# Kernel optimization log

Measured on AMD Instinct MI355X. Metric: run time of the kernel, lower is better.

## Reference

```python
import jax, jax.numpy as jnp
from jax import lax
import numpy as np

NUM_EMBEDDINGS = 8192
EMBEDDING_DIM = 256
COMMITMENT_COST = 0.25


def setup_inputs() -> dict:
    key = jax.random.key(0)
    k1, k2 = jax.random.split(key)
    z = jax.random.normal(k1, (16, EMBEDDING_DIM, 32, 32), dtype=jnp.float32)
    codebook = jax.random.uniform(
        k2, (NUM_EMBEDDINGS, EMBEDDING_DIM), dtype=jnp.float32,
        minval=-1.0 / NUM_EMBEDDINGS, maxval=1.0 / NUM_EMBEDDINGS)
    return {"z": z, "codebook": codebook}


def reference(z, codebook):
    B, C, H, W = z.shape  # C == embedding_dim
    zp = jnp.transpose(z, (0, 2, 3, 1))          # [B, H, W, C]
    z_flat = zp.reshape(-1, C)                    # [N, C], N = B*H*W
    # squared-distance via ||z||^2 + ||e||^2 - 2 z.e
    z2 = jnp.sum(z_flat * z_flat, axis=1, keepdims=True)   # [N, 1]
    e2 = jnp.sum(codebook * codebook, axis=1)               # [K]
    ez = z_flat @ codebook.T                                # [N, K]
    distances = z2 + e2 - 2.0 * ez                          # [N, K]
    e_indices = jnp.argmin(distances, axis=1)               # [N]
    z_q = codebook[e_indices]                               # [N, C]
    # Faithfully reproduce the original's mislabeled unpack:
    # torch does B, D, H, W = z.shape on the BHWC tensor, then
    # z_q.view(B, H, W, D).permute(0, 3, 1, 2) == reshape(B, W, C, H) -> (0,3,1,2)
    z_q = jnp.transpose(z_q.reshape(B, W, C, H), (0, 3, 1, 2))  # [B, H, W, C]
    commitment_loss = jnp.mean((lax.stop_gradient(zp) - z_q) ** 2)
    codebook_loss = jnp.mean((zp - lax.stop_gradient(z_q)) ** 2)
    loss = codebook_loss + COMMITMENT_COST * commitment_loss
    z_q_st = zp + lax.stop_gradient(z_q - zp)   # straight-through, [B, H, W, C]
    return z_q_st, loss, e_indices
```

## Files before the change

kernel.cpp:

```cpp
#include <hip/hip_runtime.h>
#include <stdint.h>

#define NROWS 16384
#define KENT  8192
#define CDIM  256
#define NELEM 4194304

#define ZSCALE 22.0f
#define ESCALE 1040384.0f
#define MARGIN_INT 4096
#define SBIAS 4194304


typedef int v4i __attribute__((ext_vector_type(4)));

__device__ inline int q8(float x, float s) {
    int v = __float2int_rn(x * s);
    return v < -127 ? -127 : (v > 127 ? 127 : v);
}
__device__ inline unsigned pk4(int a, int b, int c, int d) {
    return (a & 255) | ((b & 255) << 8) | ((c & 255) << 16) | ((d & 255) << 24);
}
__device__ inline unsigned umax_(unsigned a, unsigned b) { return a > b ? a : b; }
__device__ inline unsigned umin_(unsigned a, unsigned b) { return a < b ? a : b; }
__device__ inline void gload_lds16(const void* g, void* l) {
    __builtin_amdgcn_global_load_lds(
        (const __attribute__((address_space(1))) void*)g,
        (__attribute__((address_space(3))) void*)l, 16, 0, 0);
}

__global__ __launch_bounds__(128) void vq_prep(
        const float* __restrict__ z, const float* __restrict__ cb,
        float* __restrict__ z2w, char* __restrict__ zbi8,
        char* __restrict__ cbbi8, float* __restrict__ loss_out) {
    const int t = threadIdx.x;
    const int bid = blockIdx.x;

    if (bid >= 256) {
        const int p = bid - 256, n0 = p * 128;
        char* dst = cbbi8 + p * 32768;
        const float* src = cb + (n0 + t) * 256;
#pragma unroll
        for (int q = 0; q < 16; ++q) {
            float4 a = *(const float4*)(src + q * 16);
            float4 b = *(const float4*)(src + q * 16 + 4);
            float4 c = *(const float4*)(src + q * 16 + 8);
            float4 d = *(const float4*)(src + q * 16 + 12);
            uint4 v;
            v.x = pk4(q8(a.x,ESCALE), q8(a.y,ESCALE), q8(a.z,ESCALE), q8(a.w,ESCALE));
            v.y = pk4(q8(b.x,ESCALE), q8(b.y,ESCALE), q8(b.z,ESCALE), q8(b.w,ESCALE));
            v.z = pk4(q8(c.x,ESCALE), q8(c.y,ESCALE), q8(c.z,ESCALE), q8(c.w,ESCALE));
            v.w = pk4(q8(d.x,ESCALE), q8(d.y,ESCALE), q8(d.z,ESCALE), q8(d.w,ESCALE));
            *(uint4*)&dst[(q * 128 + t) * 16] = v;
        }
        if (p == 0 && t == 0) loss_out[0] = 0.f;
        return;
    }

    __shared__ float s64[64];
    const int r = t & 63;
    const int blk = t >> 6;
    const int n = bid * 64 + r;
    const int b = n >> 10, hw = n & 1023;
    const float* base = z + b * 262144 + hw;

    const int p = n >> 7, rp = n & 127;
    char* dst = zbi8 + p * 32768;

    float t0[16], p01[16], p0123[16], C[16];

#pragma unroll
    for (int j = 0; j < 8; ++j) {
        float a[16];
#pragma unroll
        for (int L = 0; L < 16; ++L)
            a[L] = base[(blk * 128 + L + 16 * j) * 1024];
        int qb[16];
#pragma unroll
        for (int L = 0; L < 16; ++L) {
            qb[L] = q8(a[L], ZSCALE);
            float sq = a[L] * a[L];
            asm volatile("" : "+v"(sq));
            if (j == 0 || j == 2 || j == 4 || j == 6) t0[L] = sq;
            else if (j == 1) p01[L] = t0[L] + sq;
            else if (j == 3) p0123[L] = p01[L] + (t0[L] + sq);
            else if (j == 5) p01[L] = t0[L] + sq;
            else             C[L] = p0123[L] + (p01[L] + (t0[L] + sq));
        }
        uint4 v;
        v.x = pk4(qb[0], qb[1], qb[2], qb[3]);
        v.y = pk4(qb[4], qb[5], qb[6], qb[7]);
        v.z = pk4(qb[8], qb[9], qb[10], qb[11]);
        v.w = pk4(qb[12], qb[13], qb[14], qb[15]);
        *(uint4*)&dst[((blk * 8 + j) * 128 + rp) * 16] = v;
    }
    float t8[8];
#pragma unroll
    for (int L = 0; L < 8; ++L) t8[L] = C[L] + C[L + 8];
    float t4[4];
#pragma unroll
    for (int L = 0; L < 4; ++L) t4[L] = t8[L] + t8[L + 4];
    float t2a = t4[0] + t4[2];
    float t2b = t4[1] + t4[3];
    float bs = t2a + t2b;

    if (blk == 1) s64[r] = bs;
    __syncthreads();
    if (blk == 0) z2w[n] = bs + s64[r];
}

__global__ __launch_bounds__(256, 4) void vq_gemm(
        const char* __restrict__ zbi8,
        const char* __restrict__ cbbi8,
        unsigned long long* __restrict__ gstats) {
    __shared__ __align__(16) char smem[32768];

    const int tid = threadIdx.x;
    const int w = tid >> 6, l = tid & 63;
    const int q4 = l >> 4, cl = l & 15;
    const int mw = w & 1, nw = w >> 1;

    const unsigned bx = blockIdx.x;
    const unsigned xcd = bx & 7, local = bx >> 3;
    const unsigned png = local >> 8;
    const unsigned rem = local & 255;
    const unsigned pm = (rem >> 4) * 8 + xcd;
    const unsigned pn = png * 16 + (rem & 15);

    const char* Ab = zbi8 + pm * 32768;
    const char* Bb = cbbi8 + pn * 32768;

#pragma unroll
    for (int u = 0; u < 8; ++u)
        gload_lds16(Ab + u * 4096 + tid * 16, smem + u * 4096 + (w << 10));

    const char* abase = Bb + (q4 * 128 + mw * 64 + cl) * 16;
    v4i af[4], afn[4];
#pragma unroll
    for (int i = 0; i < 4; ++i)
        af[i] = *(const v4i*)(abase + i * 256);

    const unsigned vb = ((unsigned)SBIAS << 6) + (unsigned)(q4 * 4);

    v4i acc[4][4];
    __syncthreads();

#pragma unroll
    for (int kt = 0; kt < 4; ++kt) {
        v4i bfl[4];
#pragma unroll
        for (int j = 0; j < 4; ++j)
            bfl[j] = *(const v4i*)(smem + kt * 8192 + q4 * 2048
                                        + nw * 1024 + j * 256 + cl * 16);
        if (kt < 3) {
#pragma unroll
            for (int i = 0; i < 4; ++i)
                afn[i] = *(const v4i*)(abase + (kt + 1) * 8192 + i * 256);
        }
#pragma unroll
        for (int i = 0; i < 4; ++i)
#pragma unroll
            for (int j = 0; j < 4; ++j) {
                if (kt == 0)
                    acc[i][j] = __builtin_amdgcn_mfma_i32_16x16x64_i8(
                        af[i], bfl[j], (v4i)0, 0, 0, 0);
                else
                    acc[i][j] = __builtin_amdgcn_mfma_i32_16x16x64_i8(
                        af[i], bfl[j], acc[i][j], 0, 0, 0);
            }
#pragma unroll
        for (int i = 0; i < 4; ++i) af[i] = afn[i];
    }

    unsigned long long* gs = gstats + (pn * 2 + (unsigned)mw) * 16384u
                                    + pm * 128u + (unsigned)(nw * 64);
#pragma unroll
    for (int jj = 0; jj < 4; ++jj) {
        unsigned m1[8], m2[8];
#pragma unroll
        for (int i = 0; i < 4; ++i)
#pragma unroll
            for (int gp = 0; gp < 2; ++gp) {
                unsigned pa = ((unsigned)acc[i][jj][2 * gp] << 6)
                              + vb + (unsigned)(i * 16 + 2 * gp);
                unsigned pb = ((unsigned)acc[i][jj][2 * gp + 1] << 6)
                              + vb + (unsigned)(i * 16 + 2 * gp + 1);
                m1[i * 2 + gp] = umax_(pa, pb);
                m2[i * 2 + gp] = umin_(pa, pb);
            }
#pragma unroll
        for (int s = 4; s >= 1; s >>= 1)
#pragma unroll
            for (int u = 0; u < 4; ++u) {
                if (u < s) {
                    unsigned a1 = m1[u], a2 = m2[u];
                    unsigned b1 = m1[u + s], b2 = m2[u + s];
                    m1[u] = umax_(a1, b1);
                    m2[u] = umax_(umin_(a1, b1), umax_(a2, b2));
                }
            }
        unsigned t1 = m1[0], t2 = m2[0];
#pragma unroll
        for (int off = 16; off <= 32; off <<= 1) {
            unsigned o1 = (unsigned)__shfl_xor((int)t1, off);
            unsigned o2 = (unsigned)__shfl_xor((int)t2, off);
            t2 = umax_(umax_(t2, o2), umin_(t1, o1));
            t1 = umax_(t1, o1);
        }
        if (q4 == 0)
            gs[jj * 16 + cl] =
                ((unsigned long long)t1 << 32) | (unsigned long long)t2;
    }
}

__global__ __launch_bounds__(256) void vq_finalize(
        const float* __restrict__ z, const float* __restrict__ cb,
        const float* __restrict__ z2w,
        const unsigned long long* __restrict__ gstats,
        float* __restrict__ out, float* __restrict__ out_idx) {
    __shared__ float zs[32][32];
    __shared__ unsigned pmax[8][32];
    __shared__ int thrL[32];
    __shared__ unsigned candL[512];
    __shared__ unsigned blkcnt;
    __shared__ unsigned long long bestL[32];
    __shared__ float tile[32 * 257];

    const int t = threadIdx.x;
    const int bid = blockIdx.x;
    const int n0 = bid * 32;
    const int b = bid >> 5, j = bid & 31;
    const int hw0 = j * 32;
    const int r = t & 31, gc = t >> 5;

    unsigned long long e[16];
    unsigned m = 0;
#pragma unroll
    for (int g2 = 0; g2 < 16; ++g2) {
        e[g2] = gstats[(size_t)(gc * 16 + g2) * 16384u + (unsigned)(n0 + r)];
        m = umax_(m, (unsigned)(e[g2] >> 32));
    }
    pmax[gc][r] = m;
    if (t == 0) blkcnt = 0;
    __syncthreads();
    if (t < 32) {
        unsigned mm = 0;
#pragma unroll
        for (int g = 0; g < 8; ++g) mm = umax_(mm, pmax[g][t]);
        thrL[t] = (int)(mm >> 6) - MARGIN_INT;
        bestL[t] = ~0ull;
    }
    __syncthreads();

    {
        int th = thrL[r];
#pragma unroll
        for (int g2 = 0; g2 < 16; ++g2) {
            unsigned p1 = (unsigned)(e[g2] >> 32), p2 = (unsigned)e[g2];
            unsigned kb = (unsigned)(gc * 16 + g2) * 64u;
            if ((int)(p1 >> 6) >= th) {
                unsigned pos = atomicAdd(&blkcnt, 1u);
                if (pos < 512u)
                    candL[pos] = ((unsigned)r << 13) | (kb + (p1 & 63u));
            }
            if ((int)(p2 >> 6) >= th) {
                unsigned pos = atomicAdd(&blkcnt, 1u);
                if (pos < 512u)
                    candL[pos] = ((unsigned)r << 13) | (kb + (p2 & 63u));
            }
        }
    }
    __syncthreads();
    int ns = (int)(blkcnt < 512u ? blkcnt : 512u);

    for (int base = 0; base < ns; base += 256) {
        bool active = base + t < ns;
        int rr0 = 0, k = 0;
        if (active) {
            unsigned v = candL[base + t];
            rr0 = v >> 13; k = v & 8191;
        }
        float sacc = 0.f;
        for (int ch = 0; ch < 8; ++ch) {
            __syncthreads();
            {
                int rr = t & 31, cc2 = t >> 5;
#pragma unroll
                for (int u = 0; u < 4; ++u) {
                    int cc = u * 8 + cc2;
                    zs[cc][rr] = z[b * 262144 + (ch * 32 + cc) * 1024 + hw0 + rr];
                }
            }
            __syncthreads();
            if (active) {
                const float4* cbp = (const float4*)(cb + k * 256 + ch * 32);
                float4 A0 = cbp[0], A1 = cbp[1], A2 = cbp[2], A3 = cbp[3];
                float4 A4 = cbp[4], A5 = cbp[5], A6 = cbp[6], A7 = cbp[7];
                float Af[32] = {A0.x,A0.y,A0.z,A0.w, A1.x,A1.y,A1.z,A1.w,
                                A2.x,A2.y,A2.z,A2.w, A3.x,A3.y,A3.z,A3.w,
                                A4.x,A4.y,A4.z,A4.w, A5.x,A5.y,A5.z,A5.w,
                                A6.x,A6.y,A6.z,A6.w, A7.x,A7.y,A7.z,A7.w};
#pragma unroll
                for (int u = 0; u < 32; ++u)
                    sacc = __builtin_fmaf(zs[u][rr0], Af[u], sacc);
            }
        }
        if (active) {
            float d = z2w[n0 + rr0] - 2.0f * sacc;
            unsigned long long key =
                ((unsigned long long)__float_as_uint(d) << 32) | (unsigned)k;
            atomicMin(&bestL[rr0], key);
        }
    }
    __syncthreads();
    if (t < 32)
        out_idx[n0 + t] = (float)(unsigned)(bestL[t] & 0xFFFFFFFFu);

    {
        const int c0 = t & 63;
        const int w0 = (t >> 6) * 8;
#pragma unroll
        for (int it = 0; it < 8; ++it) {
            int wr = w0 + it;
            int kk = (int)(unsigned)(bestL[wr] & 0xFFFFFFFFu);
            const float* src = cb + kk * 256 + c0;
            float* drow = tile + wr * 257 + c0;
            drow[0]   = src[0];
            drow[64]  = src[64];
            drow[128] = src[128];
            drow[192] = src[192];
        }
    }
    __syncthreads();

    float* obase = out + b * 262144 + j * 256;
    const int wv = t >> 3, cb8 = (t & 7) * 32;
#pragma unroll
    for (int it = 0; it < 32; ++it)
        obase[it * 8192 + t] = tile[wv * 257 + cb8 + it];
}

__global__ __launch_bounds__(256) void vq_loss(
        const float* __restrict__ z, const float* __restrict__ out,
        float* __restrict__ loss_out) {
    __shared__ float zs[256][33];
    __shared__ float wsum[4];

    const int t = threadIdx.x;
    const int b = blockIdx.x >> 5, i = blockIdx.x & 31;

#pragma unroll
    for (int it = 0; it < 32; ++it) {
        int k = it * 8 + (t >> 5);
        zs[k][t & 31] = z[b * 262144 + k * 1024 + i * 32 + (t & 31)];
    }
    __syncthreads();

    const float* ob = out + b * 262144 + i * 8192;
    float lsum = 0.f;
#pragma unroll 4
    for (int it = 0; it < 32; ++it) {
        float d = zs[t][it] - ob[it * 256 + t];
        lsum = __builtin_fmaf(d, d, lsum);
    }
#pragma unroll
    for (int off = 32; off >= 1; off >>= 1) lsum += __shfl_down(lsum, off, 64);
    int lane = t & 63, wv = t >> 6;
    if (lane == 0) wsum[wv] = lsum;
    __syncthreads();
    if (t == 0)
        atomicAdd(loss_out, (wsum[0] + wsum[1] + wsum[2] + wsum[3]) *
                            (1.25f / (float)NELEM));
}

extern "C" void kernel_launch(void* const* d_in, const int* in_sizes, int n_in,
                              void* d_out, int out_size, void* d_ws, size_t ws_size,
                              hipStream_t stream) {
    const float* z  = (const float*)d_in[0];
    const float* cb = (const float*)d_in[1];
    float* out = (float*)d_out;

    char* ws = (char*)d_ws;
    char* zbi8               = ws;
    char* cbbi8              = ws + 4194304;
    unsigned long long* gstats = (unsigned long long*)(ws + 6291456);
    float* z2w               = (float*)(ws + 23068672);

    vq_prep<<<320, 128, 0, stream>>>(z, cb, z2w, zbi8, cbbi8, out + NELEM);

    vq_gemm<<<8192, 256, 0, stream>>>(zbi8, cbbi8, gstats);

    vq_finalize<<<512, 256, 0, stream>>>(z, cb, z2w, gstats,
                                         out, out + NELEM + 1);

    vq_loss<<<512, 256, 0, stream>>>(z, out, out + NELEM);
}
```

Measured before the change: 153.0 us.

## Widen prep and loss grids, preload z tile in finalize, raise MFMA priority

vq_prep now runs 768 blocks of 256 threads. Each z row is split across more threads, and the partial squared sums are combined through shared memory. vq_loss doubles its block count by halving the columns each block handles. vq_finalize loads the full 256x32 z tile into LDS once up front, which removes the per-chunk syncthreads reloads in the candidate rescoring loop. The GEMM wraps its MFMA block in s_setprio to favor math issue. Together these aim for more parallelism and fewer barriers, at the cost of extra shared memory and a changed summation order for z2.

```diff
diff --git a/kernel.cpp b/kernel.cpp
--- a/kernel.cpp
+++ b/kernel.cpp
@@ -29,19 +29,23 @@
         (__attribute__((address_space(3))) void*)l, 16, 0, 0);
 }
 
-__global__ __launch_bounds__(128) void vq_prep(
+__global__ __launch_bounds__(256) void vq_prep(
         const float* __restrict__ z, const float* __restrict__ cb,
         float* __restrict__ z2w, char* __restrict__ zbi8,
         char* __restrict__ cbbi8, float* __restrict__ loss_out) {
     const int t = threadIdx.x;
     const int bid = blockIdx.x;
 
-    if (bid >= 256) {
-        const int p = bid - 256, n0 = p * 128;
+    if (bid >= 512) {
+        const int ppi = bid - 512;
+        const int r5 = t & 31, qp = t >> 5;
+        const int row = ppi * 32 + r5;
+        const int p = row >> 7, rowp = row & 127;
         char* dst = cbbi8 + p * 32768;
-        const float* src = cb + (n0 + t) * 256;
-#pragma unroll
-        for (int q = 0; q < 16; ++q) {
+        const float* src = cb + row * 256;
+#pragma unroll
+        for (int qq = 0; qq < 2; ++qq) {
+            const int q = qp * 2 + qq;
             float4 a = *(const float4*)(src + q * 16);
             float4 b = *(const float4*)(src + q * 16 + 4);
             float4 c = *(const float4*)(src + q * 16 + 8);
@@ -51,26 +55,29 @@
             v.y = pk4(q8(b.x,ESCALE), q8(b.y,ESCALE), q8(b.z,ESCALE), q8(b.w,ESCALE));
             v.z = pk4(q8(c.x,ESCALE), q8(c.y,ESCALE), q8(c.z,ESCALE), q8(c.w,ESCALE));
             v.w = pk4(q8(d.x,ESCALE), q8(d.y,ESCALE), q8(d.z,ESCALE), q8(d.w,ESCALE));
-            *(uint4*)&dst[(q * 128 + t) * 16] = v;
-        }
-        if (p == 0 && t == 0) loss_out[0] = 0.f;
+            *(uint4*)&dst[(q * 128 + rowp) * 16] = v;
+        }
+        if (ppi == 0 && t == 0) loss_out[0] = 0.f;
         return;
     }
 
-    __shared__ float s64[64];
-    const int r = t & 63;
-    const int blk = t >> 6;
-    const int n = bid * 64 + r;
+    __shared__ float pp[2][4][32][17];
+    __shared__ float s32[32];
+    const int r = t & 31;
+    const int part = t >> 5;
+    const int blk = part >> 2, jp = part & 3;
+    const int n = bid * 32 + r;
     const int b = n >> 10, hw = n & 1023;
     const float* base = z + b * 262144 + hw;
 
     const int p = n >> 7, rp = n & 127;
     char* dst = zbi8 + p * 32768;
 
-    float t0[16], p01[16], p0123[16], C[16];
-
-#pragma unroll
-    for (int j = 0; j < 8; ++j) {
+    float t0[16], p01[16];
+
+#pragma unroll
+    for (int jj2 = 0; jj2 < 2; ++jj2) {
+        const int j = jp * 2 + jj2;
         float a[16];
 #pragma unroll
         for (int L = 0; L < 16; ++L)
@@ -81,11 +88,8 @@
             qb[L] = q8(a[L], ZSCALE);
             float sq = a[L] * a[L];
             asm volatile("" : "+v"(sq));
-            if (j == 0 || j == 2 || j == 4 || j == 6) t0[L] = sq;
-            else if (j == 1) p01[L] = t0[L] + sq;
-            else if (j == 3) p0123[L] = p01[L] + (t0[L] + sq);
-            else if (j == 5) p01[L] = t0[L] + sq;
-            else             C[L] = p0123[L] + (p01[L] + (t0[L] + sq));
+            if (jj2 == 0) t0[L] = sq;
+            else          p01[L] = t0[L] + sq;
         }
         uint4 v;
         v.x = pk4(qb[0], qb[1], qb[2], qb[3]);
@@ -94,19 +98,32 @@
         v.w = pk4(qb[12], qb[13], qb[14], qb[15]);
         *(uint4*)&dst[((blk * 8 + j) * 128 + rp) * 16] = v;
     }
-    float t8[8];
-#pragma unroll
-    for (int L = 0; L < 8; ++L) t8[L] = C[L] + C[L + 8];
-    float t4[4];
-#pragma unroll
-    for (int L = 0; L < 4; ++L) t4[L] = t8[L] + t8[L + 4];
-    float t2a = t4[0] + t4[2];
-    float t2b = t4[1] + t4[3];
-    float bs = t2a + t2b;
-
-    if (blk == 1) s64[r] = bs;
-    __syncthreads();
-    if (blk == 0) z2w[n] = bs + s64[r];
+
+#pragma unroll
+    for (int L = 0; L < 16; ++L) pp[blk][jp][r][L] = p01[L];
+    __syncthreads();
+    float bs = 0.f;
+    if (jp == 0) {
+        float C[16];
+#pragma unroll
+        for (int L = 0; L < 16; ++L) {
+            float p0123 = pp[blk][0][r][L] + pp[blk][1][r][L];
+            float p4567 = pp[blk][2][r][L] + pp[blk][3][r][L];
+            C[L] = p0123 + p4567;
+        }
+        float t8[8];
+#pragma unroll
+        for (int L = 0; L < 8; ++L) t8[L] = C[L] + C[L + 8];
+        float t4[4];
+#pragma unroll
+        for (int L = 0; L < 4; ++L) t4[L] = t8[L] + t8[L + 4];
+        float t2a = t4[0] + t4[2];
+        float t2b = t4[1] + t4[3];
+        bs = t2a + t2b;
+        if (blk == 1) s32[r] = bs;
+    }
+    __syncthreads();
+    if (part == 0) z2w[n] = bs + s32[r];
 }
 
 __global__ __launch_bounds__(256, 4) void vq_gemm(
@@ -157,6 +174,7 @@
             for (int i = 0; i < 4; ++i)
                 afn[i] = *(const v4i*)(abase + (kt + 1) * 8192 + i * 256);
         }
+        __builtin_amdgcn_s_setprio(1);
 #pragma unroll
         for (int i = 0; i < 4; ++i)
 #pragma unroll
@@ -168,6 +186,7 @@
                     acc[i][j] = __builtin_amdgcn_mfma_i32_16x16x64_i8(
                         af[i], bfl[j], acc[i][j], 0, 0, 0);
             }
+        __builtin_amdgcn_s_setprio(0);
 #pragma unroll
         for (int i = 0; i < 4; ++i) af[i] = afn[i];
     }
@@ -218,7 +237,7 @@
         const float* __restrict__ z2w,
         const unsigned long long* __restrict__ gstats,
         float* __restrict__ out, float* __restrict__ out_idx) {
-    __shared__ float zs[32][32];
+    __shared__ float zs[256][32];
     __shared__ unsigned pmax[8][32];
     __shared__ int thrL[32];
     __shared__ unsigned candL[512];
@@ -232,6 +251,15 @@
     const int b = bid >> 5, j = bid & 31;
     const int hw0 = j * 32;
     const int r = t & 31, gc = t >> 5;
+
+    {
+        const int rr = t & 31, cc2 = t >> 5;
+#pragma unroll
+        for (int u = 0; u < 32; ++u) {
+            int cc = u * 8 + cc2;
+            zs[cc][rr] = z[b * 262144 + cc * 1024 + hw0 + rr];
+        }
+    }
 
     unsigned long long e[16];
     unsigned m = 0;
@@ -274,25 +302,12 @@
     int ns = (int)(blkcnt < 512u ? blkcnt : 512u);
 
     for (int base = 0; base < ns; base += 256) {
-        bool active = base + t < ns;
-        int rr0 = 0, k = 0;
-        if (active) {
+        if (base + t < ns) {
             unsigned v = candL[base + t];
-            rr0 = v >> 13; k = v & 8191;
-        }
-        float sacc = 0.f;
-        for (int ch = 0; ch < 8; ++ch) {
-            __syncthreads();
-            {
-                int rr = t & 31, cc2 = t >> 5;
-#pragma unroll
-                for (int u = 0; u < 4; ++u) {
-                    int cc = u * 8 + cc2;
-                    zs[cc][rr] = z[b * 262144 + (ch * 32 + cc) * 1024 + hw0 + rr];
-                }
-            }
-            __syncthreads();
-            if (active) {
+            int rr0 = v >> 13, k = v & 8191;
+            float sacc = 0.f;
+#pragma unroll 1
+            for (int ch = 0; ch < 8; ++ch) {
                 const float4* cbp = (const float4*)(cb + k * 256 + ch * 32);
                 float4 A0 = cbp[0], A1 = cbp[1], A2 = cbp[2], A3 = cbp[3];
                 float4 A4 = cbp[4], A5 = cbp[5], A6 = cbp[6], A7 = cbp[7];
@@ -302,10 +317,8 @@
                                 A6.x,A6.y,A6.z,A6.w, A7.x,A7.y,A7.z,A7.w};
 #pragma unroll
                 for (int u = 0; u < 32; ++u)
-                    sacc = __builtin_fmaf(zs[u][rr0], Af[u], sacc);
-            }
-        }
-        if (active) {
+                    sacc = __builtin_fmaf(zs[ch * 32 + u][rr0], Af[u], sacc);
+            }
             float d = z2w[n0 + rr0] - 2.0f * sacc;
             unsigned long long key =
                 ((unsigned long long)__float_as_uint(d) << 32) | (unsigned)k;
@@ -343,23 +356,25 @@
 __global__ __launch_bounds__(256) void vq_loss(
         const float* __restrict__ z, const float* __restrict__ out,
         float* __restrict__ loss_out) {
-    __shared__ float zs[256][33];
+    __shared__ float zs[256][17];
     __shared__ float wsum[4];
 
     const int t = threadIdx.x;
-    const int b = blockIdx.x >> 5, i = blockIdx.x & 31;
-
-#pragma unroll
-    for (int it = 0; it < 32; ++it) {
-        int k = it * 8 + (t >> 5);
-        zs[k][t & 31] = z[b * 262144 + k * 1024 + i * 32 + (t & 31)];
-    }
-    __syncthreads();
-
-    const float* ob = out + b * 262144 + i * 8192;
+    const int bid = blockIdx.x;
+    const int b = bid >> 6, rest = bid & 63;
+    const int i = rest >> 1, jh = rest & 1;
+
+#pragma unroll
+    for (int it = 0; it < 16; ++it) {
+        int k = it * 16 + (t >> 4);
+        zs[k][t & 15] = z[b * 262144 + k * 1024 + i * 32 + jh * 16 + (t & 15)];
+    }
+    __syncthreads();
+
+    const float* ob = out + b * 262144 + i * 8192 + jh * 16 * 256;
     float lsum = 0.f;
 #pragma unroll 4
-    for (int it = 0; it < 32; ++it) {
+    for (int it = 0; it < 16; ++it) {
         float d = zs[t][it] - ob[it * 256 + t];
         lsum = __builtin_fmaf(d, d, lsum);
     }
@@ -386,12 +401,12 @@
     unsigned long long* gstats = (unsigned long long*)(ws + 6291456);
     float* z2w               = (float*)(ws + 23068672);
 
-    vq_prep<<<320, 128, 0, stream>>>(z, cb, z2w, zbi8, cbbi8, out + NELEM);
+    vq_prep<<<768, 256, 0, stream>>>(z, cb, z2w, zbi8, cbbi8, out + NELEM);
 
     vq_gemm<<<8192, 256, 0, stream>>>(zbi8, cbbi8, gstats);
 
     vq_finalize<<<512, 256, 0, stream>>>(z, cb, z2w, gstats,
                                          out, out + NELEM + 1);
 
-    vq_loss<<<512, 256, 0, stream>>>(z, out, out + NELEM);
-}
+    vq_loss<<<1024, 256, 0, stream>>>(z, out, out + NELEM);
+}
```

After: 152.7 us. Within noise of the previous version (-0.2%).
